# Kernel optimization log

Hardware: AMD Instinct MI355X
Metric: run time of the kernel (lower is better)

Reference implementation:

```python
import jax, jax.numpy as jnp
import numpy as np

NB, NC, IN, HID, OUT, ENG = 8, 16384, 64, 128, 64, 128
SYNC, DEBATE = 0.15, 0.15


def setup_inputs() -> dict:
    key = jax.random.key(0)
    ks = jax.random.split(key, 24)
    rn = lambda k, s, sc=0.05: jax.random.normal(k, s, jnp.float32) * sc
    return {
        "x": jax.random.normal(ks[0], (1, IN), jnp.float32),
        "noise": jax.random.normal(ks[1], (NB, 1, IN), jnp.float32),
        "amps": jax.random.uniform(ks[2], (NB,), jnp.float32, 0.5, 1.5),
        "hiddens": jax.random.normal(ks[3], (NB, NC, HID), jnp.float32) * 0.1,
        "eaW1": rn(ks[4], (ENG, IN + HID)), "eaB1": rn(ks[5], (ENG,)),
        "eaW2": rn(ks[6], (OUT, ENG)), "eaB2": rn(ks[7], (OUT,)),
        "egW1": rn(ks[8], (ENG, IN + HID)), "egB1": rn(ks[9], (ENG,)),
        "egW2": rn(ks[10], (OUT, ENG)), "egB2": rn(ks[11], (OUT,)),
        "gru_Wih": rn(ks[12], (3 * HID, OUT + 1)), "gru_Whh": rn(ks[13], (3 * HID, HID)),
        "gru_bih": rn(ks[14], (3 * HID,)), "gru_bhh": rn(ks[15], (3 * HID,)),
        "headW": rn(ks[16], (IN, OUT)), "headb": rn(ks[17], (IN,)),
        "mixW": rn(ks[18], (HID, HID * NB)), "mixb": rn(ks[19], (HID,)),
        "step": 10,
    }


def reference(x, noise, amps, hiddens, eaW1, eaB1, eaW2, eaB2,
              egW1, egB1, egW2, egB2, gru_Wih, gru_Whh, gru_bih, gru_bhh,
              headW, headb, mixW, mixb, step):
    sg = jax.lax.stop_gradient
    # per-branch perturbed input, broadcast over cells
    scale = 0.05 * jnp.arange(1, NB + 1, dtype=x.dtype)[:, None, None]
    xb = jnp.broadcast_to(x[None] + noise * scale, (NB, NC, IN))
    comb = jnp.concatenate([xb, hiddens], axis=-1)          # (NB,NC,IN+HID)
    a = jax.nn.relu(comb @ eaW1.T + eaB1) @ eaW2.T + eaB2
    g = jax.nn.relu(comb @ egW1.T + egB1) @ egW2.T + egB2
    out = a - g                                             # (NB,NC,OUT)
    tension = jnp.mean(out ** 2, axis=-1)                   # (NB,NC)

    # GRUCell update (mem input is detached in the original)
    mem_in = sg(jnp.concatenate([out, tension[..., None]], axis=-1))
    gi = mem_in @ gru_Wih.T + gru_bih                       # (NB,NC,3H)
    gh = hiddens @ gru_Whh.T + gru_bhh
    ir, iz, inn = jnp.split(gi, 3, axis=-1)
    hr, hz, hn = jnp.split(gh, 3, axis=-1)
    r = jax.nn.sigmoid(ir + hr)
    z = jax.nn.sigmoid(iz + hz)
    n = jnp.tanh(inn + r * hn)
    newh = sg((1.0 - z) * n + z * hiddens)                  # stored detached

    # faction sync + debate (state only)
    nf = min(8, NC // 2)
    fs = NC // nf
    core = newh[:, :nf * fs].reshape(NB, nf, fs, HID)
    core = (1.0 - SYNC) * core + SYNC * core.mean(axis=2, keepdims=True)
    if step > 5:
        glob = core.mean(axis=2).mean(axis=1)               # (NB,HID)
        dc = max(1, fs // 4)
        core = core.at[:, :, :dc].set(
            (1.0 - DEBATE) * core[:, :, :dc] + DEBATE * glob[:, None, None, :])
    newh = jnp.concatenate([core.reshape(NB, nf * fs, HID), newh[:, nf * fs:]], axis=1)

    # amplitude-weighted branch combine (amps used via .item() -> constants)
    aabs = jnp.abs(amps)
    aabs = aabs / (aabs.sum() + 1e-8)
    cell_out = jnp.einsum('b,bnd->nd', sg(aabs), out)       # (NC,OUT)
    avg_t = tension.mean(axis=0)                            # (NC,)
    w = jax.nn.softmax(sg(avg_t))                           # weights from .item()'d tensions
    combined = (w[:, None] * cell_out).sum(axis=0, keepdims=True)  # (1,OUT)
    pred = combined @ headW.T + headb                       # (1,IN)

    # interference mixer state update on branch 0
    interf = newh.mean(axis=1).reshape(1, -1) @ mixW.T + mixb       # (1,HID)
    newh = newh.at[0].add(sg(interf) * 0.05)

    return pred, avg_t.mean(), newh
```

## Files before the change

### kernel.cpp

```cpp
#include <hip/hip_runtime.h>
#include <math.h>

#define NB   8
#define NCC  16384
#define HID  128

typedef __attribute__((ext_vector_type(8))) short short8;
typedef __attribute__((ext_vector_type(4))) float f32x4;

#define MFMA(a,b,c) __builtin_amdgcn_mfma_f32_16x16x32_bf16(a,b,c,0,0,0)

#define WS_AABS   0
#define WS_BASE1  8
#define WS_BOUT   2056
#define WS_BSUMR  2120
#define WS_BSUMZ  2248
#define WS_BIHN   2376
#define WS_BHHN   2504
#define WS_W64    2632
#define WS_STAT   3016
#define WS_INTERF 3024
#define WS_FRAG   3152
#define WS_SD     64592
#define WS_HM     72784
#define WS_AVGT   73808
#define WS_TS     90192
#define WS_FMEAN  221264
#define WS_GLOB   229456
#define WS_PART2  230480
#define WS_FPART  246864
#define WS_CO     771152


__device__ __forceinline__ unsigned short f2b(float f) {
    unsigned int u = __float_as_uint(f);
    unsigned int r = (u + 0x7fffu + ((u >> 16) & 1u)) >> 16;
    return (unsigned short)r;
}
__device__ __forceinline__ float b2f(unsigned short us) {
    return __uint_as_float(((unsigned int)us) << 16);
}
__device__ __forceinline__ float sigm(float x) {
    return __builtin_amdgcn_rcpf(1.f + __expf(-x));
}
__device__ __forceinline__ float tanh_fast(float x) {
    return 1.f - 2.f * __builtin_amdgcn_rcpf(__expf(2.f * x) + 1.f);
}
__device__ __forceinline__ void stg(char* dst, int row, int cb, float4 u, float4 v) {
    unsigned int p0 = (unsigned)f2b(u.x) | ((unsigned)f2b(u.y) << 16);
    unsigned int p1 = (unsigned)f2b(u.z) | ((unsigned)f2b(u.w) << 16);
    unsigned int p2 = (unsigned)f2b(v.x) | ((unsigned)f2b(v.y) << 16);
    unsigned int p3 = (unsigned)f2b(v.z) | ((unsigned)f2b(v.w) << 16);
    uint4 pk = make_uint4(p0, p1, p2, p3);
    *(uint4*)(dst + row * 256 + (cb ^ ((row & 7) << 4))) = pk;
}

__global__ __launch_bounds__(256) void k0s(
    const float* __restrict__ x, const float* __restrict__ noise,
    const float* __restrict__ amps,
    const float* __restrict__ eaW1, const float* __restrict__ eaB1,
    const float* __restrict__ egW1, const float* __restrict__ egB1,
    const float* __restrict__ eaB2, const float* __restrict__ egB2,
    const float* __restrict__ gbih, const float* __restrict__ gbhh,
    const float* __restrict__ gWih, float* __restrict__ ws)
{
    __shared__ float xb[8][64];
    int t = threadIdx.x;
    for (int i = t; i < 512; i += 256) {
        int b = i >> 6, k = i & 63;
        xb[b][k] = x[k] + noise[b * 64 + k] * (0.05f * (float)(b + 1));
    }
    if (t == 0) {
        float s = 0.f;
        for (int b = 0; b < 8; b++) s += fabsf(amps[b]);
        s += 1e-8f;
        for (int b = 0; b < 8; b++) ws[WS_AABS + b] = fabsf(amps[b]) / s;
    }
    __syncthreads();
    for (int i = t; i < 2048; i += 256) {
        int b = i >> 8, n = i & 255;
        const float* Wp; float s;
        if (n < 128) { Wp = eaW1 + n * 192; s = eaB1[n]; }
        else         { Wp = egW1 + (n - 128) * 192; s = egB1[n - 128]; }
        for (int k = 0; k < 64; k++) s += xb[b][k] * Wp[k];
        ws[WS_BASE1 + i] = s;
    }
    if (t < 64) ws[WS_BOUT + t] = eaB2[t] - egB2[t];
    if (t < 128) {
        ws[WS_BSUMR + t] = gbih[t] + gbhh[t];
        ws[WS_BSUMZ + t] = gbih[128 + t] + gbhh[128 + t];
        ws[WS_BIHN + t]  = gbih[256 + t];
        ws[WS_BHHN + t]  = gbhh[256 + t];
    }
    for (int i = t; i < 384; i += 256) ws[WS_W64 + i] = gWih[i * 65 + 64];
}

__global__ __launch_bounds__(1024) void kfrag(
    const float* __restrict__ eaW1, const float* __restrict__ egW1,
    const float* __restrict__ eaW2, const float* __restrict__ egW2,
    const float* __restrict__ gWih, const float* __restrict__ gWhh,
    float* __restrict__ ws)
{
    int i = blockIdx.x * 1024 + threadIdx.x;
    if (i >= 122880) return;
    short* wsh = (short*)(ws + WS_FRAG);
    float v;
    if (i < 32768) {
        int rel = i;
        int j = rel & 7, l = (rel >> 3) & 63, tk = rel >> 9;
        int kt = tk & 3, nt = tk >> 2;
        int n = nt * 16 + (l & 15), k = kt * 32 + ((l >> 4) << 3) + j;
        v = (n < 128) ? eaW1[n * 192 + 64 + k] : egW1[(n - 128) * 192 + 64 + k];
    } else if (i < 49152) {
        int rel = i - 32768;
        int j = rel & 7, l = (rel >> 3) & 63, tk = rel >> 9;
        int kt = tk & 7, nt = tk >> 3;
        int d = nt * 16 + (l & 15), k = kt * 32 + ((l >> 4) << 3) + j;
        v = (k < 128) ? eaW2[d * 128 + k] : -egW2[d * 128 + (k - 128)];
    } else if (i < 73728) {
        int rel = i - 49152;
        int j = rel & 7, l = (rel >> 3) & 63, tk = rel >> 9;
        int kt = tk & 1, nt = tk >> 1;
        int r = nt * 16 + (l & 15), k = kt * 32 + ((l >> 4) << 3) + j;
        v = gWih[r * 65 + k];
    } else {
        int rel = i - 73728;
        int j = rel & 7, l = (rel >> 3) & 63, tk = rel >> 9;
        int kt = tk & 3, nt = tk >> 2;
        int r = nt * 16 + (l & 15), k = kt * 32 + ((l >> 4) << 3) + j;
        v = gWhh[r * 128 + k];
    }
    wsh[i] = (short)f2b(v);
}

__global__ __launch_bounds__(512) void kA(
    const float* __restrict__ hiddens, float* __restrict__ newh,
    float* __restrict__ ws)
{
    __shared__ char  wlds[98304];
    __shared__ char  hsb[64 * 256];
    __shared__ char  agb[64 * 512];
    __shared__ float ts_s[64];
    __shared__ float tsum_s[64];

    const int t    = threadIdx.x;
    const int lane = t & 63;
    const int w    = t >> 6;
    const int rh   = w >> 2;
    const int nq   = w & 3;
    const int col  = lane & 15;
    const int kq   = lane >> 4;
    const int r0   = rh * 32;
    const int n0   = blockIdx.x * 64;

    {
        const float4* src = (const float4*)(ws + WS_FRAG);
        float4* dst = (float4*)wlds;
#pragma unroll
        for (int p = 0; p < 12; p++) dst[p * 512 + t] = src[p * 512 + t];
    }
    const short8* W1F = (const short8*)wlds;
    const short8* W2F = (const short8*)(wlds + 65536);

    const float bo = ws[WS_BOUT + nq * 16 + col];
    float co_reg[8];
#pragma unroll
    for (int i = 0; i < 8; i++) co_reg[i] = 0.f;
    if (t < 64) tsum_s[t] = 0.f;

    const int flat0 = t * 8;
    const int flat1 = (512 + t) * 8;
    const int srow0 = flat0 >> 7, scb0 = (flat0 & 127) * 2;
    const int srow1 = flat1 >> 7, scb1 = (flat1 & 127) * 2;

    {
        const float* hs = hiddens + (size_t)n0 * HID;
        float4 a0 = *(const float4*)(hs + flat0);
        float4 a1 = *(const float4*)(hs + flat0 + 4);
        float4 c0 = *(const float4*)(hs + flat1);
        float4 c1 = *(const float4*)(hs + flat1 + 4);
        stg(hsb, srow0, scb0, a0, a1);
        stg(hsb, srow1, scb1, c0, c1);
    }
    float4 pfa0, pfa1, pfb0, pfb1;
    unsigned short* outu = (unsigned short*)newh;

    for (int b = 0; b < NB; ++b) {
        __syncthreads();
        if (t < 64) {
            if (b > 0) {
                ws[WS_TS + (size_t)(b - 1) * NCC + n0 + t] = ts_s[t];
                tsum_s[t] += ts_s[t];
            }
            ts_s[t] = 0.f;
        }

        if (b < 7) {
            const float* hsn = hiddens + ((size_t)((b + 1) * NCC + n0)) * HID;
            pfa0 = *(const float4*)(hsn + flat0);
            pfa1 = *(const float4*)(hsn + flat0 + 4);
            pfb0 = *(const float4*)(hsn + flat1);
            pfb1 = *(const float4*)(hsn + flat1 + 4);
        }

        {
            short8 aH[2][4];
#pragma unroll
            for (int mt = 0; mt < 2; mt++)
#pragma unroll
                for (int ks = 0; ks < 4; ks++) {
                    int row = r0 + mt * 16 + col;
                    aH[mt][ks] = *(const short8*)(hsb + row * 256 +
                                   ((ks * 64 + (kq << 4)) ^ ((row & 7) << 4)));
                }
#pragma unroll
            for (int nti = 0; nti < 4; nti++) {
                int nt = nq * 4 + nti;
                f32x4 ac0 = {0.f, 0.f, 0.f, 0.f};
                f32x4 ac1 = {0.f, 0.f, 0.f, 0.f};
#pragma unroll
                for (int kt = 0; kt < 4; kt++) {
                    short8 bf = W1F[(nt * 4 + kt) * 64 + lane];
                    ac0 = MFMA(aH[0][kt], bf, ac0);
                    ac1 = MFMA(aH[1][kt], bf, ac1);
                }
                int n = nt * 16 + col;
                float bs = ws[WS_BASE1 + b * 256 + n];
#pragma unroll
                for (int mt = 0; mt < 2; mt++) {
                    f32x4 a = mt ? ac1 : ac0;
#pragma unroll
                    for (int j = 0; j < 4; j++) {
                        int row = r0 + mt * 16 + (kq << 2) + j;
                        float v = fmaxf(a[j] + bs, 0.f);
                        *(unsigned short*)(agb + row * 512 +
                            ((n * 2) ^ ((row & 7) << 4))) = f2b(v);
                    }
                }
            }
        }
        __syncthreads();

        if (b < 7) {
            stg(hsb, srow0, scb0, pfa0, pfa1);
            stg(hsb, srow1, scb1, pfb0, pfb1);
        }

        {
            f32x4 ov0 = {0.f, 0.f, 0.f, 0.f};
            f32x4 ov1 = {0.f, 0.f, 0.f, 0.f};
#pragma unroll
            for (int kt = 0; kt < 8; kt++) {
                int kb = kt * 64 + (kq << 4);
                int ra = r0 + col, rb = r0 + 16 + col;
                short8 a0 = *(const short8*)(agb + ra * 512 + (kb ^ ((ra & 7) << 4)));
                short8 a1 = *(const short8*)(agb + rb * 512 + (kb ^ ((rb & 7) << 4)));
                short8 bf = W2F[(nq * 8 + kt) * 64 + lane];
                ov0 = MFMA(a0, bf, ov0);
                ov1 = MFMA(a1, bf, ov1);
            }
            int d = nq * 16 + col;
            float aab = ws[WS_AABS + b];
#pragma unroll
            for (int mt = 0; mt < 2; mt++) {
                f32x4 ov = mt ? ov1 : ov0;
#pragma unroll
                for (int j = 0; j < 4; j++) {
                    int row = r0 + mt * 16 + (kq << 2) + j;
                    float v = ov[j] + bo;
                    co_reg[mt * 4 + j] += aab * v;
                    outu[(size_t)(b * NCC + n0 + row) * 256 + 192 + d] = f2b(v);
                    float sq = v * v;
                    sq += __shfl_xor(sq, 1);
                    sq += __shfl_xor(sq, 2);
                    sq += __shfl_xor(sq, 4);
                    sq += __shfl_xor(sq, 8);
                    if (col == 0) atomicAdd(&ts_s[row], sq);
                }
            }
        }
    }
    __syncthreads();
    if (t < 64) {
        ws[WS_TS + (size_t)7 * NCC + n0 + t] = ts_s[t];
        tsum_s[t] += ts_s[t];
        ws[WS_AVGT + n0 + t] = tsum_s[t] * (1.f / 512.f);
    }
    {
        int d = nq * 16 + col;
#pragma unroll
        for (int mt = 0; mt < 2; mt++)
#pragma unroll
            for (int j = 0; j < 4; j++) {
                int row = r0 + mt * 16 + (kq << 2) + j;
                ws[WS_CO + (size_t)(n0 + row) * 64 + d] = co_reg[mt * 4 + j];
            }
    }
}

__global__ __launch_bounds__(512) void kB(
    const float* __restrict__ hiddens, float* __restrict__ newh,
    float* __restrict__ ws)
{
    __shared__ char  wl[147456];
    __shared__ char  hsb[32 * 256];
    __shared__ char  otb[32 * 128];
    __shared__ float ts_s[32];
    __shared__ float fp2[2][128];

    const int t    = threadIdx.x;
    const int lane = t & 63;
    const int w    = t >> 6;
    const int rh   = w >> 2;
    const int nq   = w & 3;
    const int col  = lane & 15;
    const int kq   = lane >> 4;
    const int chunk = blockIdx.x;
    const int n0   = chunk * 32;

    {
        const float4* src = (const float4*)(ws + WS_FRAG) + 6144;
        float4* dst = (float4*)wl;
#pragma unroll
        for (int p = 0; p < 18; p++) dst[p * 512 + t] = src[p * 512 + t];
    }
    const short8* WIHF = (const short8*)wl;
    const short8* WHHF = (const short8*)(wl + 49152);
    const unsigned short* outu = (const unsigned short*)newh;

    float bsrH[2], bszH[2], binH[2], bhnH[2], wrH[2], wzH[2], wnH[2];
#pragma unroll
    for (int hgi = 0; hgi < 2; hgi++) {
        int h = nq * 32 + hgi * 16 + col;
        bsrH[hgi] = ws[WS_BSUMR + h];
        bszH[hgi] = ws[WS_BSUMZ + h];
        binH[hgi] = ws[WS_BIHN + h];
        bhnH[hgi] = ws[WS_BHHN + h];
        wrH[hgi]  = ws[WS_W64 + h];
        wzH[hgi]  = ws[WS_W64 + 128 + h];
        wnH[hgi]  = ws[WS_W64 + 256 + h];
    }

    const int flat = t * 8;
    const int srow = t >> 4;
    const int scb  = (t & 15) * 16;
    const int ocell = t >> 4;
    const int ooff  = (t & 15) * 4;

    float4 rh0, rh1;
    uint2  ro;
    float  rts = 0.f;
    {
        const float* hs = hiddens + (size_t)n0 * HID;
        rh0 = *(const float4*)(hs + flat);
        rh1 = *(const float4*)(hs + flat + 4);
        ro  = *(const uint2*)(outu + (size_t)(n0 + ocell) * 256 + 192 + ooff);
        if (t < 32) rts = ws[WS_TS + n0 + t];
    }

    for (int b = 0; b < NB; ++b) {
        stg(hsb, srow, scb, rh0, rh1);
        *(uint2*)(otb + ocell * 128 + ((ooff * 2) ^ ((ocell & 7) << 4))) = ro;
        if (t < 32) ts_s[t] = rts;
        __syncthreads();

        if (b < 7) {
            const float* hsn = hiddens + ((size_t)((b + 1) * NCC + n0)) * HID;
            rh0 = *(const float4*)(hsn + flat);
            rh1 = *(const float4*)(hsn + flat + 4);
            ro  = *(const uint2*)(outu + (size_t)((b + 1) * NCC + n0 + ocell) * 256 + 192 + ooff);
            if (t < 32) rts = ws[WS_TS + (size_t)(b + 1) * NCC + n0 + t];
        }

        {
            float* nbase = newh + ((size_t)(b * NCC + n0)) * HID;
            const int ra = rh * 16 + col;
#pragma unroll
            for (int hgi = 0; hgi < 2; hgi++) {
                int hg = nq * 2 + hgi;
                f32x4 R = {0.f,0.f,0.f,0.f};
                f32x4 Z = {0.f,0.f,0.f,0.f};
                f32x4 I = {0.f,0.f,0.f,0.f};
                f32x4 N = {0.f,0.f,0.f,0.f};
#pragma unroll
                for (int ks = 0; ks < 2; ks++) {
                    short8 a0 = *(const short8*)(otb + ra * 128 +
                                 ((ks * 64 + (kq << 4)) ^ ((ra & 7) << 4)));
                    R = MFMA(a0, WIHF[(hg * 2 + ks) * 64 + lane], R);
                    Z = MFMA(a0, WIHF[((hg + 8) * 2 + ks) * 64 + lane], Z);
                    I = MFMA(a0, WIHF[((hg + 16) * 2 + ks) * 64 + lane], I);
                }
#pragma unroll
                for (int ks = 0; ks < 4; ks++) {
                    short8 a0 = *(const short8*)(hsb + ra * 256 +
                                 ((ks * 64 + (kq << 4)) ^ ((ra & 7) << 4)));
                    R = MFMA(a0, WHHF[(hg * 4 + ks) * 64 + lane], R);
                    Z = MFMA(a0, WHHF[((hg + 8) * 4 + ks) * 64 + lane], Z);
                    N = MFMA(a0, WHHF[((hg + 16) * 4 + ks) * 64 + lane], N);
                }
                int h = hg * 16 + col;
                float flsum = 0.f;
#pragma unroll
                for (int j = 0; j < 4; j++) {
                    int row = rh * 16 + (kq << 2) + j;
                    float tv = ts_s[row] * (1.f / 64.f);
                    float r  = sigm(R[j] + bsrH[hgi] + tv * wrH[hgi]);
                    float z  = sigm(Z[j] + bszH[hgi] + tv * wzH[hgi]);
                    float hn = N[j] + bhnH[hgi];
                    float nn = tanh_fast(I[j] + binH[hgi] + tv * wnH[hgi] + r * hn);
                    float hold = b2f(*(const unsigned short*)(hsb + row * 256 +
                                     ((h * 2) ^ ((row & 7) << 4))));
                    float nh = (1.f - z) * nn + z * hold;
                    nbase[(size_t)row * HID + h] = nh;
                    flsum += nh;
                }
                flsum += __shfl_xor(flsum, 16);
                flsum += __shfl_xor(flsum, 32);
                if (kq == 0) fp2[rh][h] = flsum;
            }
        }
        __syncthreads();

        if (t < 128)
            ws[WS_FPART + ((size_t)(b * 512 + chunk)) * 128 + t] = fp2[0][t] + fp2[1][t];
    }
}

__global__ __launch_bounds__(128) void k2_fmean(float* __restrict__ ws)
{
    int bf = blockIdx.x;
    int b = bf >> 3, f = bf & 7;
    int h = threadIdx.x;
    float s = 0.f, s8 = 0.f;
    for (int j = 0; j < 64; j++) {
        float v = ws[WS_FPART + ((size_t)(b * 512 + f * 64 + j)) * 128 + h];
        s += v;
        if (j < 16) s8 += v;
    }
    ws[WS_FMEAN + (b * 8 + f) * 128 + h] = s * (1.f / 2048.f);
    ws[WS_SD + (b * 8 + f) * 128 + h] = s8;
}

__global__ __launch_bounds__(1024) void k2_glob(float* __restrict__ ws)
{
    int t = threadIdx.x;
    int b = t >> 7, h = t & 127;
    float s = 0.f;
    for (int f = 0; f < 8; f++) s += ws[WS_FMEAN + (b * 8 + f) * 128 + h];
    ws[WS_GLOB + t] = s * 0.125f;
}

__global__ __launch_bounds__(1024) void k4hm(
    const int* __restrict__ step, float* __restrict__ ws)
{
    int t = threadIdx.x;
    int b = t >> 7, h = t & 127;
    float gl = ws[WS_GLOB + b * 128 + h];
    float tot = 16384.f * gl;
    if (step[0] > 5) {
        float sd = 0.f;
        for (int f = 0; f < 8; f++) sd += ws[WS_SD + (b * 8 + f) * 128 + h];
        float extra = 3481.6f * gl - 0.85f * sd;
        tot += 0.15f * extra;
    }
    ws[WS_HM + t] = tot * (1.f / 16384.f);
}

__global__ __launch_bounds__(256) void k4mv(
    const float* __restrict__ mixW, const float* __restrict__ mixb,
    float* __restrict__ ws)
{
    __shared__ float red[256];
    int h = blockIdx.x, t = threadIdx.x;
    float4 wv = *(const float4*)(mixW + (size_t)h * 1024 + t * 4);
    float4 hv = *(const float4*)(ws + WS_HM + t * 4);
    float s = wv.x * hv.x + wv.y * hv.y + wv.z * hv.z + wv.w * hv.w;
    red[t] = s; __syncthreads();
    for (int st = 128; st > 0; st >>= 1) { if (t < st) red[t] += red[t + st]; __syncthreads(); }
    if (t == 0) ws[WS_INTERF + h] = mixb[h] + red[0];
}

__global__ __launch_bounds__(256) void k35_blend(
    float* __restrict__ newh, const float* __restrict__ ws,
    const int* __restrict__ step)
{
    int blk = blockIdx.x;
    int b = blk >> 8, ck = blk & 255;
    int t = threadIdx.x;
    int h = t & 127, half = t >> 7;
    int base = ck * 64 + half * 32;
    int f = ck >> 5;
    bool deb = (step[0] > 5) && (((ck * 64) & 2047) < 512);
    float fm  = ws[WS_FMEAN + (b * 8 + f) * 128 + h];
    float gl  = ws[WS_GLOB + b * 128 + h];
    float itf = (b == 0) ? 0.05f * ws[WS_INTERF + h] : 0.f;
    for (int i = 0; i < 32; i++) {
        size_t idx = ((size_t)b * NCC + base + i) * HID + h;
        float v = newh[idx];
        v = 0.85f * v + 0.15f * fm;
        if (deb) v = 0.85f * v + 0.15f * gl;
        newh[idx] = v + itf;
    }
}

__global__ __launch_bounds__(1024) void kstat(float* __restrict__ ws, float* __restrict__ d_out)
{
    __shared__ float red[1024];
    __shared__ float msh;
    int t = threadIdx.x;
    float mx = -3.4e38f, sm = 0.f;
    for (int n = t; n < NCC; n += 1024) {
        float v = ws[WS_AVGT + n];
        mx = fmaxf(mx, v);
        sm += v;
    }
    red[t] = mx; __syncthreads();
    for (int st = 512; st > 0; st >>= 1) { if (t < st) red[t] = fmaxf(red[t], red[t + st]); __syncthreads(); }
    if (t == 0) msh = red[0];
    __syncthreads();
    float m = msh;
    red[t] = sm; __syncthreads();
    for (int st = 512; st > 0; st >>= 1) { if (t < st) red[t] += red[t + st]; __syncthreads(); }
    if (t == 0) d_out[64] = red[0] * (1.f / (float)NCC);
    __syncthreads();
    float se = 0.f;
    for (int n = t; n < NCC; n += 1024) se += __expf(ws[WS_AVGT + n] - m);
    red[t] = se; __syncthreads();
    for (int st = 512; st > 0; st >>= 1) { if (t < st) red[t] += red[t + st]; __syncthreads(); }
    if (t == 0) { ws[WS_STAT] = m; ws[WS_STAT + 1] = red[0]; }
}

__global__ __launch_bounds__(256) void kred(float* __restrict__ ws)
{
    __shared__ float wexp[64];
    __shared__ float red[256];
    int blk = blockIdx.x, t = threadIdx.x;
    int n0 = blk * 64;
    float m = ws[WS_STAT];
    if (t < 64) wexp[t] = __expf(ws[WS_AVGT + n0 + t] - m);
    __syncthreads();
    int d = t & 63, q = t >> 6;
    float s = 0.f;
    for (int i = 0; i < 16; i++) {
        int c = q * 16 + i;
        s += wexp[c] * ws[WS_CO + (size_t)(n0 + c) * 64 + d];
    }
    red[t] = s; __syncthreads();
    if (t < 64)
        ws[WS_PART2 + blk * 64 + t] = red[t] + red[64 + t] + red[128 + t] + red[192 + t];
}

__global__ __launch_bounds__(256) void kpred(
    const float* __restrict__ headW, const float* __restrict__ headb,
    float* __restrict__ ws, float* __restrict__ d_out)
{
    __shared__ float red[256];
    __shared__ float comb[64];
    int t = threadIdx.x;
    int d = t & 63, q = t >> 6;
    float s = 0.f;
    for (int i = 0; i < 64; i++) s += ws[WS_PART2 + (q * 64 + i) * 64 + d];
    red[t] = s; __syncthreads();
    if (t < 64) comb[t] = (red[t] + red[64 + t] + red[128 + t] + red[192 + t]) / ws[WS_STAT + 1];
    __syncthreads();
    if (t < 64) {
        float p = headb[t];
        for (int d2 = 0; d2 < 64; d2++) p += comb[d2] * headW[t * 64 + d2];
        d_out[t] = p;
    }
}

extern "C" void kernel_launch(void* const* d_in, const int* in_sizes, int n_in,
                              void* d_out, int out_size, void* d_ws, size_t ws_size,
                              hipStream_t stream)
{
    const float* x       = (const float*)d_in[0];
    const float* noise   = (const float*)d_in[1];
    const float* amps    = (const float*)d_in[2];
    const float* hiddens = (const float*)d_in[3];
    const float* eaW1    = (const float*)d_in[4];
    const float* eaB1    = (const float*)d_in[5];
    const float* eaW2    = (const float*)d_in[6];
    const float* eaB2    = (const float*)d_in[7];
    const float* egW1    = (const float*)d_in[8];
    const float* egB1    = (const float*)d_in[9];
    const float* egW2    = (const float*)d_in[10];
    const float* egB2    = (const float*)d_in[11];
    const float* gWih    = (const float*)d_in[12];
    const float* gWhh    = (const float*)d_in[13];
    const float* gbih    = (const float*)d_in[14];
    const float* gbhh    = (const float*)d_in[15];
    const float* headW   = (const float*)d_in[16];
    const float* headb   = (const float*)d_in[17];
    const float* mixW    = (const float*)d_in[18];
    const float* mixb    = (const float*)d_in[19];
    const int*   step    = (const int*)d_in[20];

    float* out  = (float*)d_out;
    float* newh = out + 65;
    float* ws   = (float*)d_ws;

    k0s<<<1, 256, 0, stream>>>(x, noise, amps, eaW1, eaB1, egW1, egB1,
                               eaB2, egB2, gbih, gbhh, gWih, ws);
    kfrag<<<120, 1024, 0, stream>>>(eaW1, egW1, eaW2, egW2, gWih, gWhh, ws);
    kA<<<256, 512, 0, stream>>>(hiddens, newh, ws);
    kB<<<512, 512, 0, stream>>>(hiddens, newh, ws);
    k2_fmean<<<64, 128, 0, stream>>>(ws);
    k2_glob<<<1, 1024, 0, stream>>>(ws);
    k4hm<<<1, 1024, 0, stream>>>(step, ws);
    k4mv<<<128, 256, 0, stream>>>(mixW, mixb, ws);
    k35_blend<<<2048, 256, 0, stream>>>(newh, ws, step);
    kstat<<<1, 1024, 0, stream>>>(ws, out);
    kred<<<256, 256, 0, stream>>>(ws);
    kpred<<<1, 256, 0, stream>>>(headW, headb, ws, out);
}
```

Baseline: 142.6 us.

## Double block size in kA/kB to 1024 threads and fuse glob/hm kernels

kA and kB move from 512 to 1024 threads per block, so each wave handles half the rows or head columns and per-thread MFMA work and register footprint shrink. Each wave keeps one accumulator set instead of two. In kB the staging loads are limited to the first 512 threads. The separate global-mean and hm kernels are merged into one launch to save a dispatch. The aim is more waves per CU to hide latency, at the cost of less register-level reuse of loaded fragments and heavier per-block synchronisation.

```diff
diff --git a/kernel.cpp b/kernel.cpp
--- a/kernel.cpp
+++ b/kernel.cpp
@@ -30,7 +30,6 @@
 #define WS_PART2  230480
 #define WS_FPART  246864
 #define WS_CO     771152
-
 
 __device__ __forceinline__ unsigned short f2b(float f) {
     unsigned int u = __float_as_uint(f);
@@ -133,7 +132,7 @@
     wsh[i] = (short)f2b(v);
 }
 
-__global__ __launch_bounds__(512) void kA(
+__global__ __launch_bounds__(1024) void kA(
     const float* __restrict__ hiddens, float* __restrict__ newh,
     float* __restrict__ ws)
 {
@@ -146,43 +145,39 @@
     const int t    = threadIdx.x;
     const int lane = t & 63;
     const int w    = t >> 6;
-    const int rh   = w >> 2;
+    const int rg   = w >> 2;
     const int nq   = w & 3;
     const int col  = lane & 15;
     const int kq   = lane >> 4;
-    const int r0   = rh * 32;
+    const int r0   = rg * 16;
     const int n0   = blockIdx.x * 64;
 
     {
         const float4* src = (const float4*)(ws + WS_FRAG);
         float4* dst = (float4*)wlds;
 #pragma unroll
-        for (int p = 0; p < 12; p++) dst[p * 512 + t] = src[p * 512 + t];
+        for (int p = 0; p < 6; p++) dst[p * 1024 + t] = src[p * 1024 + t];
     }
     const short8* W1F = (const short8*)wlds;
     const short8* W2F = (const short8*)(wlds + 65536);
 
     const float bo = ws[WS_BOUT + nq * 16 + col];
-    float co_reg[8];
-#pragma unroll
-    for (int i = 0; i < 8; i++) co_reg[i] = 0.f;
+    float co_reg[4];
+#pragma unroll
+    for (int i = 0; i < 4; i++) co_reg[i] = 0.f;
     if (t < 64) tsum_s[t] = 0.f;
 
-    const int flat0 = t * 8;
-    const int flat1 = (512 + t) * 8;
-    const int srow0 = flat0 >> 7, scb0 = (flat0 & 127) * 2;
-    const int srow1 = flat1 >> 7, scb1 = (flat1 & 127) * 2;
+    const int flat = t * 8;
+    const int srow = flat >> 7;
+    const int scb  = (flat & 127) * 2;
 
     {
         const float* hs = hiddens + (size_t)n0 * HID;
-        float4 a0 = *(const float4*)(hs + flat0);
-        float4 a1 = *(const float4*)(hs + flat0 + 4);
-        float4 c0 = *(const float4*)(hs + flat1);
-        float4 c1 = *(const float4*)(hs + flat1 + 4);
-        stg(hsb, srow0, scb0, a0, a1);
-        stg(hsb, srow1, scb1, c0, c1);
-    }
-    float4 pfa0, pfa1, pfb0, pfb1;
+        float4 a0 = *(const float4*)(hs + flat);
+        float4 a1 = *(const float4*)(hs + flat + 4);
+        stg(hsb, srow, scb, a0, a1);
+    }
+    float4 pfa0, pfa1;
     unsigned short* outu = (unsigned short*)newh;
 
     for (int b = 0; b < NB; ++b) {
@@ -194,89 +189,65 @@
             }
             ts_s[t] = 0.f;
         }
-
         if (b < 7) {
             const float* hsn = hiddens + ((size_t)((b + 1) * NCC + n0)) * HID;
-            pfa0 = *(const float4*)(hsn + flat0);
-            pfa1 = *(const float4*)(hsn + flat0 + 4);
-            pfb0 = *(const float4*)(hsn + flat1);
-            pfb1 = *(const float4*)(hsn + flat1 + 4);
+            pfa0 = *(const float4*)(hsn + flat);
+            pfa1 = *(const float4*)(hsn + flat + 4);
         }
 
         {
-            short8 aH[2][4];
-#pragma unroll
-            for (int mt = 0; mt < 2; mt++)
-#pragma unroll
-                for (int ks = 0; ks < 4; ks++) {
-                    int row = r0 + mt * 16 + col;
-                    aH[mt][ks] = *(const short8*)(hsb + row * 256 +
-                                   ((ks * 64 + (kq << 4)) ^ ((row & 7) << 4)));
-                }
+            short8 aH[4];
+#pragma unroll
+            for (int ks = 0; ks < 4; ks++) {
+                int row = r0 + col;
+                aH[ks] = *(const short8*)(hsb + row * 256 +
+                           ((ks * 64 + (kq << 4)) ^ ((row & 7) << 4)));
+            }
 #pragma unroll
             for (int nti = 0; nti < 4; nti++) {
                 int nt = nq * 4 + nti;
-                f32x4 ac0 = {0.f, 0.f, 0.f, 0.f};
-                f32x4 ac1 = {0.f, 0.f, 0.f, 0.f};
-#pragma unroll
-                for (int kt = 0; kt < 4; kt++) {
-                    short8 bf = W1F[(nt * 4 + kt) * 64 + lane];
-                    ac0 = MFMA(aH[0][kt], bf, ac0);
-                    ac1 = MFMA(aH[1][kt], bf, ac1);
-                }
+                f32x4 ac = {0.f, 0.f, 0.f, 0.f};
+#pragma unroll
+                for (int kt = 0; kt < 4; kt++)
+                    ac = MFMA(aH[kt], W1F[(nt * 4 + kt) * 64 + lane], ac);
                 int n = nt * 16 + col;
                 float bs = ws[WS_BASE1 + b * 256 + n];
 #pragma unroll
-                for (int mt = 0; mt < 2; mt++) {
-                    f32x4 a = mt ? ac1 : ac0;
-#pragma unroll
-                    for (int j = 0; j < 4; j++) {
-                        int row = r0 + mt * 16 + (kq << 2) + j;
-                        float v = fmaxf(a[j] + bs, 0.f);
-                        *(unsigned short*)(agb + row * 512 +
-                            ((n * 2) ^ ((row & 7) << 4))) = f2b(v);
-                    }
+                for (int j = 0; j < 4; j++) {
+                    int row = r0 + (kq << 2) + j;
+                    float v = fmaxf(ac[j] + bs, 0.f);
+                    *(unsigned short*)(agb + row * 512 +
+                        ((n * 2) ^ ((row & 7) << 4))) = f2b(v);
                 }
             }
         }
         __syncthreads();
 
-        if (b < 7) {
-            stg(hsb, srow0, scb0, pfa0, pfa1);
-            stg(hsb, srow1, scb1, pfb0, pfb1);
-        }
+        if (b < 7) stg(hsb, srow, scb, pfa0, pfa1);
 
         {
-            f32x4 ov0 = {0.f, 0.f, 0.f, 0.f};
-            f32x4 ov1 = {0.f, 0.f, 0.f, 0.f};
+            f32x4 ov = {0.f, 0.f, 0.f, 0.f};
 #pragma unroll
             for (int kt = 0; kt < 8; kt++) {
                 int kb = kt * 64 + (kq << 4);
-                int ra = r0 + col, rb = r0 + 16 + col;
+                int ra = r0 + col;
                 short8 a0 = *(const short8*)(agb + ra * 512 + (kb ^ ((ra & 7) << 4)));
-                short8 a1 = *(const short8*)(agb + rb * 512 + (kb ^ ((rb & 7) << 4)));
-                short8 bf = W2F[(nq * 8 + kt) * 64 + lane];
-                ov0 = MFMA(a0, bf, ov0);
-                ov1 = MFMA(a1, bf, ov1);
+                ov = MFMA(a0, W2F[(nq * 8 + kt) * 64 + lane], ov);
             }
             int d = nq * 16 + col;
             float aab = ws[WS_AABS + b];
 #pragma unroll
-            for (int mt = 0; mt < 2; mt++) {
-                f32x4 ov = mt ? ov1 : ov0;
-#pragma unroll
-                for (int j = 0; j < 4; j++) {
-                    int row = r0 + mt * 16 + (kq << 2) + j;
-                    float v = ov[j] + bo;
-                    co_reg[mt * 4 + j] += aab * v;
-                    outu[(size_t)(b * NCC + n0 + row) * 256 + 192 + d] = f2b(v);
-                    float sq = v * v;
-                    sq += __shfl_xor(sq, 1);
-                    sq += __shfl_xor(sq, 2);
-                    sq += __shfl_xor(sq, 4);
-                    sq += __shfl_xor(sq, 8);
-                    if (col == 0) atomicAdd(&ts_s[row], sq);
-                }
+            for (int j = 0; j < 4; j++) {
+                int row = r0 + (kq << 2) + j;
+                float v = ov[j] + bo;
+                co_reg[j] += aab * v;
+                outu[(size_t)(b * NCC + n0 + row) * 256 + 192 + d] = f2b(v);
+                float sq = v * v;
+                sq += __shfl_xor(sq, 1);
+                sq += __shfl_xor(sq, 2);
+                sq += __shfl_xor(sq, 4);
+                sq += __shfl_xor(sq, 8);
+                if (col == 0) atomicAdd(&ts_s[row], sq);
             }
         }
     }
@@ -289,16 +260,14 @@
     {
         int d = nq * 16 + col;
 #pragma unroll
-        for (int mt = 0; mt < 2; mt++)
-#pragma unroll
-            for (int j = 0; j < 4; j++) {
-                int row = r0 + mt * 16 + (kq << 2) + j;
-                ws[WS_CO + (size_t)(n0 + row) * 64 + d] = co_reg[mt * 4 + j];
-            }
-    }
-}
-
-__global__ __launch_bounds__(512) void kB(
+        for (int j = 0; j < 4; j++) {
+            int row = r0 + (kq << 2) + j;
+            ws[WS_CO + (size_t)(n0 + row) * 64 + d] = co_reg[j];
+        }
+    }
+}
+
+__global__ __launch_bounds__(1024) void kB(
     const float* __restrict__ hiddens, float* __restrict__ newh,
     float* __restrict__ ws)
 {
@@ -311,8 +280,8 @@
     const int t    = threadIdx.x;
     const int lane = t & 63;
     const int w    = t >> 6;
-    const int rh   = w >> 2;
-    const int nq   = w & 3;
+    const int rh   = w >> 3;
+    const int hg   = w & 7;
     const int col  = lane & 15;
     const int kq   = lane >> 4;
     const int chunk = blockIdx.x;
@@ -322,102 +291,97 @@
         const float4* src = (const float4*)(ws + WS_FRAG) + 6144;
         float4* dst = (float4*)wl;
 #pragma unroll
-        for (int p = 0; p < 18; p++) dst[p * 512 + t] = src[p * 512 + t];
+        for (int p = 0; p < 9; p++) dst[p * 1024 + t] = src[p * 1024 + t];
     }
     const short8* WIHF = (const short8*)wl;
     const short8* WHHF = (const short8*)(wl + 49152);
     const unsigned short* outu = (const unsigned short*)newh;
 
-    float bsrH[2], bszH[2], binH[2], bhnH[2], wrH[2], wzH[2], wnH[2];
-#pragma unroll
-    for (int hgi = 0; hgi < 2; hgi++) {
-        int h = nq * 32 + hgi * 16 + col;
-        bsrH[hgi] = ws[WS_BSUMR + h];
-        bszH[hgi] = ws[WS_BSUMZ + h];
-        binH[hgi] = ws[WS_BIHN + h];
-        bhnH[hgi] = ws[WS_BHHN + h];
-        wrH[hgi]  = ws[WS_W64 + h];
-        wzH[hgi]  = ws[WS_W64 + 128 + h];
-        wnH[hgi]  = ws[WS_W64 + 256 + h];
-    }
+    const int h = hg * 16 + col;
+    const float bsr = ws[WS_BSUMR + h];
+    const float bsz = ws[WS_BSUMZ + h];
+    const float bin = ws[WS_BIHN + h];
+    const float bhn = ws[WS_BHHN + h];
+    const float wr  = ws[WS_W64 + h];
+    const float wz  = ws[WS_W64 + 128 + h];
+    const float wn  = ws[WS_W64 + 256 + h];
 
     const int flat = t * 8;
-    const int srow = t >> 4;
-    const int scb  = (t & 15) * 16;
+    const int srow = flat >> 7;
+    const int scb  = (flat & 127) * 2;
     const int ocell = t >> 4;
     const int ooff  = (t & 15) * 4;
 
-    float4 rh0, rh1;
-    uint2  ro;
+    float4 rh0 = {0,0,0,0}, rh1 = {0,0,0,0};
+    uint2  ro = make_uint2(0, 0);
     float  rts = 0.f;
-    {
+    if (t < 512) {
         const float* hs = hiddens + (size_t)n0 * HID;
         rh0 = *(const float4*)(hs + flat);
         rh1 = *(const float4*)(hs + flat + 4);
         ro  = *(const uint2*)(outu + (size_t)(n0 + ocell) * 256 + 192 + ooff);
-        if (t < 32) rts = ws[WS_TS + n0 + t];
-    }
+    }
+    if (t < 32) rts = ws[WS_TS + n0 + t];
 
     for (int b = 0; b < NB; ++b) {
-        stg(hsb, srow, scb, rh0, rh1);
-        *(uint2*)(otb + ocell * 128 + ((ooff * 2) ^ ((ocell & 7) << 4))) = ro;
+        if (t < 512) {
+            stg(hsb, srow, scb, rh0, rh1);
+            *(uint2*)(otb + ocell * 128 + ((ooff * 2) ^ ((ocell & 7) << 4))) = ro;
+        }
         if (t < 32) ts_s[t] = rts;
         __syncthreads();
 
         if (b < 7) {
-            const float* hsn = hiddens + ((size_t)((b + 1) * NCC + n0)) * HID;
-            rh0 = *(const float4*)(hsn + flat);
-            rh1 = *(const float4*)(hsn + flat + 4);
-            ro  = *(const uint2*)(outu + (size_t)((b + 1) * NCC + n0 + ocell) * 256 + 192 + ooff);
+            if (t < 512) {
+                const float* hsn = hiddens + ((size_t)((b + 1) * NCC + n0)) * HID;
+                rh0 = *(const float4*)(hsn + flat);
+                rh1 = *(const float4*)(hsn + flat + 4);
+                ro  = *(const uint2*)(outu + (size_t)((b + 1) * NCC + n0 + ocell) * 256 + 192 + ooff);
+            }
             if (t < 32) rts = ws[WS_TS + (size_t)(b + 1) * NCC + n0 + t];
         }
 
         {
             float* nbase = newh + ((size_t)(b * NCC + n0)) * HID;
             const int ra = rh * 16 + col;
-#pragma unroll
-            for (int hgi = 0; hgi < 2; hgi++) {
-                int hg = nq * 2 + hgi;
-                f32x4 R = {0.f,0.f,0.f,0.f};
-                f32x4 Z = {0.f,0.f,0.f,0.f};
-                f32x4 I = {0.f,0.f,0.f,0.f};
-                f32x4 N = {0.f,0.f,0.f,0.f};
-#pragma unroll
-                for (int ks = 0; ks < 2; ks++) {
-                    short8 a0 = *(const short8*)(otb + ra * 128 +
-                                 ((ks * 64 + (kq << 4)) ^ ((ra & 7) << 4)));
-                    R = MFMA(a0, WIHF[(hg * 2 + ks) * 64 + lane], R);
-                    Z = MFMA(a0, WIHF[((hg + 8) * 2 + ks) * 64 + lane], Z);
-                    I = MFMA(a0, WIHF[((hg + 16) * 2 + ks) * 64 + lane], I);
-                }
-#pragma unroll
-                for (int ks = 0; ks < 4; ks++) {
-                    short8 a0 = *(const short8*)(hsb + ra * 256 +
-                                 ((ks * 64 + (kq << 4)) ^ ((ra & 7) << 4)));
-                    R = MFMA(a0, WHHF[(hg * 4 + ks) * 64 + lane], R);
-                    Z = MFMA(a0, WHHF[((hg + 8) * 4 + ks) * 64 + lane], Z);
-                    N = MFMA(a0, WHHF[((hg + 16) * 4 + ks) * 64 + lane], N);
-                }
-                int h = hg * 16 + col;
-                float flsum = 0.f;
-#pragma unroll
-                for (int j = 0; j < 4; j++) {
-                    int row = rh * 16 + (kq << 2) + j;
-                    float tv = ts_s[row] * (1.f / 64.f);
-                    float r  = sigm(R[j] + bsrH[hgi] + tv * wrH[hgi]);
-                    float z  = sigm(Z[j] + bszH[hgi] + tv * wzH[hgi]);
-                    float hn = N[j] + bhnH[hgi];
-                    float nn = tanh_fast(I[j] + binH[hgi] + tv * wnH[hgi] + r * hn);
-                    float hold = b2f(*(const unsigned short*)(hsb + row * 256 +
-                                     ((h * 2) ^ ((row & 7) << 4))));
-                    float nh = (1.f - z) * nn + z * hold;
-                    nbase[(size_t)row * HID + h] = nh;
-                    flsum += nh;
-                }
-                flsum += __shfl_xor(flsum, 16);
-                flsum += __shfl_xor(flsum, 32);
-                if (kq == 0) fp2[rh][h] = flsum;
-            }
+            f32x4 R = {0.f,0.f,0.f,0.f};
+            f32x4 Z = {0.f,0.f,0.f,0.f};
+            f32x4 I = {0.f,0.f,0.f,0.f};
+            f32x4 N = {0.f,0.f,0.f,0.f};
+#pragma unroll
+            for (int ks = 0; ks < 2; ks++) {
+                short8 a0 = *(const short8*)(otb + ra * 128 +
+                             ((ks * 64 + (kq << 4)) ^ ((ra & 7) << 4)));
+                R = MFMA(a0, WIHF[(hg * 2 + ks) * 64 + lane], R);
+                Z = MFMA(a0, WIHF[((hg + 8) * 2 + ks) * 64 + lane], Z);
+                I = MFMA(a0, WIHF[((hg + 16) * 2 + ks) * 64 + lane], I);
+            }
+#pragma unroll
+            for (int ks = 0; ks < 4; ks++) {
+                short8 a0 = *(const short8*)(hsb + ra * 256 +
+                             ((ks * 64 + (kq << 4)) ^ ((ra & 7) << 4)));
+                R = MFMA(a0, WHHF[(hg * 4 + ks) * 64 + lane], R);
+                Z = MFMA(a0, WHHF[((hg + 8) * 4 + ks) * 64 + lane], Z);
+                N = MFMA(a0, WHHF[((hg + 16) * 4 + ks) * 64 + lane], N);
+            }
+            float flsum = 0.f;
+#pragma unroll
+            for (int j = 0; j < 4; j++) {
+                int row = rh * 16 + (kq << 2) + j;
+                float tv = ts_s[row] * (1.f / 64.f);
+                float r  = sigm(R[j] + bsr + tv * wr);
+                float z  = sigm(Z[j] + bsz + tv * wz);
+                float hn = N[j] + bhn;
+                float nn = tanh_fast(I[j] + bin + tv * wn + r * hn);
+                float hold = b2f(*(const unsigned short*)(hsb + row * 256 +
+                                 ((h * 2) ^ ((row & 7) << 4))));
+                float nh = (1.f - z) * nn + z * hold;
+                nbase[(size_t)row * HID + h] = nh;
+                flsum += nh;
+            }
+            flsum += __shfl_xor(flsum, 16);
+            flsum += __shfl_xor(flsum, 32);
+            if (kq == 0) fp2[rh][h] = flsum;
         }
         __syncthreads();
 
@@ -441,27 +405,20 @@
     ws[WS_SD + (b * 8 + f) * 128 + h] = s8;
 }
 
-__global__ __launch_bounds__(1024) void k2_glob(float* __restrict__ ws)
+__global__ __launch_bounds__(1024) void k4gh(
+    const int* __restrict__ step, float* __restrict__ ws)
 {
     int t = threadIdx.x;
     int b = t >> 7, h = t & 127;
     float s = 0.f;
     for (int f = 0; f < 8; f++) s += ws[WS_FMEAN + (b * 8 + f) * 128 + h];
-    ws[WS_GLOB + t] = s * 0.125f;
-}
-
-__global__ __launch_bounds__(1024) void k4hm(
-    const int* __restrict__ step, float* __restrict__ ws)
-{
-    int t = threadIdx.x;
-    int b = t >> 7, h = t & 127;
-    float gl = ws[WS_GLOB + b * 128 + h];
+    float gl = s * 0.125f;
+    ws[WS_GLOB + t] = gl;
     float tot = 16384.f * gl;
     if (step[0] > 5) {
         float sd = 0.f;
         for (int f = 0; f < 8; f++) sd += ws[WS_SD + (b * 8 + f) * 128 + h];
-        float extra = 3481.6f * gl - 0.85f * sd;
-        tot += 0.15f * extra;
+        tot += 0.15f * (3481.6f * gl - 0.85f * sd);
     }
     ws[WS_HM + t] = tot * (1.f / 16384.f);
 }
@@ -603,11 +560,10 @@
     k0s<<<1, 256, 0, stream>>>(x, noise, amps, eaW1, eaB1, egW1, egB1,
                                eaB2, egB2, gbih, gbhh, gWih, ws);
     kfrag<<<120, 1024, 0, stream>>>(eaW1, egW1, eaW2, egW2, gWih, gWhh, ws);
-    kA<<<256, 512, 0, stream>>>(hiddens, newh, ws);
-    kB<<<512, 512, 0, stream>>>(hiddens, newh, ws);
+    kA<<<256, 1024, 0, stream>>>(hiddens, newh, ws);
+    kB<<<512, 1024, 0, stream>>>(hiddens, newh, ws);
     k2_fmean<<<64, 128, 0, stream>>>(ws);
-    k2_glob<<<1, 1024, 0, stream>>>(ws);
-    k4hm<<<1, 1024, 0, stream>>>(step, ws);
+    k4gh<<<1, 1024, 0, stream>>>(step, ws);
     k4mv<<<128, 256, 0, stream>>>(mixW, mixb, ws);
     k35_blend<<<2048, 256, 0, stream>>>(newh, ws, step);
     kstat<<<1, 1024, 0, stream>>>(ws, out);
```

Result: no change. 140.5 us (-1.5%).
